# Kernel optimization log

Measured on AMD Instinct MI355X. Metric: run time of the kernel, lower is better.

The kernel has to match this reference:

```python
import jax, jax.numpy as jnp
import numpy as np

N_NODES = 10000
N_EDGES = 160000
D_IN = 512
D_OUT = 512


def setup_inputs() -> dict:
    key = jax.random.key(0)
    k_x, k_e, k_wl, k_wr = jax.random.split(key, 4)
    x = jax.random.normal(k_x, (N_NODES, D_IN), dtype=jnp.float32)
    edge_index = jax.random.randint(k_e, (2, N_EDGES), 0, N_NODES, dtype=jnp.int64)
    scale = 1.0 / np.sqrt(D_IN)
    W_l = jax.random.normal(k_wl, (D_IN, D_OUT), dtype=jnp.float32) * scale
    W_r = jax.random.normal(k_wr, (D_IN, D_OUT), dtype=jnp.float32) * scale
    b = jnp.zeros((D_OUT,), dtype=jnp.float32)
    return {"x": x, "edge_index": edge_index, "W_l": W_l, "W_r": W_r, "b": b}


def reference(x, edge_index, W_l, W_r, b):
    # dropout p=0.0 -> identity
    src = edge_index[0]  # message sources (x_j)
    dst = edge_index[1]  # aggregation targets (i)
    n = x.shape[0]
    # mean neighbor aggregation: scatter-add messages, divide by in-degree
    msg = x[src]                                   # [E, D_in]
    agg = jax.ops.segment_sum(msg, dst, num_segments=n)        # [N, D_in]
    deg = jax.ops.segment_sum(jnp.ones((src.shape[0],), x.dtype), dst, num_segments=n)
    mean = agg / jnp.maximum(deg, 1.0)[:, None]
    # SAGEConv: lin_l(aggregated) + lin_r(root), bias in lin_l
    h = mean @ W_l + b + x @ W_r                   # [N, D_out]
    # Swish activation
    return h * jax.nn.sigmoid(h)
```

## Files before the change

kernel.cpp:

```cpp
#include <hip/hip_runtime.h>
#include <cstdint>
#include <cstddef>

typedef unsigned short ushort_t;
typedef __attribute__((ext_vector_type(8))) short short8;
typedef __attribute__((ext_vector_type(4))) float float4_;
typedef __attribute__((ext_vector_type(2))) float float2_;

#define GLOBAL_AS __attribute__((address_space(1)))
#define LDS_AS    __attribute__((address_space(3)))

#define D_FEAT 512
#define KDIM   1024
#define CAP    80
#define BK     128

__device__ __forceinline__ ushort_t f2bf(float f) {
    union { float f; unsigned int i; } v; v.f = f;
    unsigned int x = v.i;
    unsigned int r = (x + 0x7fffu + ((x >> 16) & 1u)) >> 16;
    return (ushort_t)r;
}

__device__ __forceinline__ void accq(float* acc, uint2 v) {
    float2_ a01 = __builtin_amdgcn_cvt_pk_f32_fp8(v.x, false);
    float2_ a23 = __builtin_amdgcn_cvt_pk_f32_fp8(v.x, true);
    float2_ a45 = __builtin_amdgcn_cvt_pk_f32_fp8(v.y, false);
    float2_ a67 = __builtin_amdgcn_cvt_pk_f32_fp8(v.y, true);
    acc[0] += a01.x; acc[1] += a01.y;
    acc[2] += a23.x; acc[3] += a23.y;
    acc[4] += a45.x; acc[5] += a45.y;
    acc[6] += a67.x; acc[7] += a67.y;
}

__global__ __launch_bounds__(256) void prep_kernel(
    const float* __restrict__ Wl, const float* __restrict__ Wr,
    const float* __restrict__ x, const int* __restrict__ ei,
    ushort_t* __restrict__ BT, ushort_t* __restrict__ xb,
    unsigned char* __restrict__ xq, unsigned int* __restrict__ cnt,
    int* __restrict__ colbuf, int N, int E, int nchunks, int cb) {
    int b = blockIdx.x;
    int t = threadIdx.x;
    if (b < cb) {
        int idx = b * 256 + t;
        if (idx >= nchunks) return;
        int row = idx >> 7;
        int c = (idx & 127) << 2;
        float4 v = *(const float4*)&x[(size_t)row * D_FEAT + c];
        ushort_t o[4] = {f2bf(v.x), f2bf(v.y), f2bf(v.z), f2bf(v.w)};
        *(uint2*)&xb[(size_t)row * D_FEAT + c] = *(const uint2*)o;
        int pk = 0;
        pk = __builtin_amdgcn_cvt_pk_fp8_f32(v.x, v.y, pk, false);
        pk = __builtin_amdgcn_cvt_pk_fp8_f32(v.z, v.w, pk, true);
        *(int*)&xq[(size_t)row * D_FEAT + c] = pk;
    } else if (b < cb + 128) {
        int bb = b - cb;
        __shared__ float tile[64][68];
        int kb = (bb & 15) * 64, nb = (bb >> 4) * 64;
#pragma unroll
        for (int ph = 0; ph < 4; ++ph) {
            int f = t * 4 + ph * 1024;
            int k = f >> 6, n = f & 63;
            int gk = kb + k;
            const float* W = (gk < 512) ? (Wl + (size_t)gk * 512 + nb + n)
                                        : (Wr + (size_t)(gk - 512) * 512 + nb + n);
            *(float4*)&tile[k][n] = *(const float4*)W;
        }
        __syncthreads();
#pragma unroll
        for (int ph = 0; ph < 4; ++ph) {
            int f = t * 4 + ph * 1024;
            int n = f >> 6, k = f & 63;
            ushort_t tmp[4];
#pragma unroll
            for (int j = 0; j < 4; ++j) tmp[j] = f2bf(tile[k + j][n]);
            *(uint2*)&BT[(size_t)(nb + n) * KDIM + kb + k] = *(const uint2*)tmp;
        }
    } else {
        int e = ((b - cb - 128) * 256 + t) * 2;
        if (e >= E) return;
        unsigned int V = cnt[N];
        int2 d2 = *(const int2*)&ei[E + e];
        int2 s2 = *(const int2*)&ei[e];
        unsigned int p0 = atomicAdd(&cnt[d2.x], 1u) - V;
        if (p0 < CAP) colbuf[(size_t)d2.x * CAP + p0] = s2.x;
        if (e + 1 < E) {
            unsigned int p1 = atomicAdd(&cnt[d2.y], 1u) - V;
            if (p1 < CAP) colbuf[(size_t)d2.y * CAP + p1] = s2.y;
        }
    }
}

__global__ __launch_bounds__(256) void agg_kernel(
    const unsigned char* __restrict__ xq, ushort_t* __restrict__ mb,
    const unsigned int* __restrict__ cnt, const int* __restrict__ colbuf,
    int n) {
    int w = threadIdx.x >> 6, l = threadIdx.x & 63;
    int node = blockIdx.x * 4 + w;
    if (node >= n) return;
    unsigned int V = cnt[n];
    int f = l << 3;
    const unsigned char* gsrc = xq + f;
    const int* bucket = colbuf + (size_t)node * CAP;
    float acc[8] = {0.f, 0.f, 0.f, 0.f, 0.f, 0.f, 0.f, 0.f};
    int deg = (int)(cnt[node] - V);
    int e = deg < CAP ? deg : CAP;
    int j = 0;
    for (; j + 7 < e; j += 8) {
        int4 i0 = *(const int4*)&bucket[j];
        int4 i1 = *(const int4*)&bucket[j + 4];
        uint2 v0 = *(const uint2*)(gsrc + (size_t)i0.x * D_FEAT);
        uint2 v1 = *(const uint2*)(gsrc + (size_t)i0.y * D_FEAT);
        uint2 v2 = *(const uint2*)(gsrc + (size_t)i0.z * D_FEAT);
        uint2 v3 = *(const uint2*)(gsrc + (size_t)i0.w * D_FEAT);
        uint2 v4 = *(const uint2*)(gsrc + (size_t)i1.x * D_FEAT);
        uint2 v5 = *(const uint2*)(gsrc + (size_t)i1.y * D_FEAT);
        uint2 v6 = *(const uint2*)(gsrc + (size_t)i1.z * D_FEAT);
        uint2 v7 = *(const uint2*)(gsrc + (size_t)i1.w * D_FEAT);
        accq(acc, v0); accq(acc, v1); accq(acc, v2); accq(acc, v3);
        accq(acc, v4); accq(acc, v5); accq(acc, v6); accq(acc, v7);
    }
    if (j + 3 < e) {
        int4 i0 = *(const int4*)&bucket[j];
        uint2 v0 = *(const uint2*)(gsrc + (size_t)i0.x * D_FEAT);
        uint2 v1 = *(const uint2*)(gsrc + (size_t)i0.y * D_FEAT);
        uint2 v2 = *(const uint2*)(gsrc + (size_t)i0.z * D_FEAT);
        uint2 v3 = *(const uint2*)(gsrc + (size_t)i0.w * D_FEAT);
        accq(acc, v0); accq(acc, v1); accq(acc, v2); accq(acc, v3);
        j += 4;
    }
    for (; j < e; ++j) {
        uint2 v0 = *(const uint2*)(gsrc + (size_t)bucket[j] * D_FEAT);
        accq(acc, v0);
    }
    float scale = 1.0f / (float)(deg > 1 ? deg : 1);
    ushort_t o[8];
#pragma unroll
    for (int k = 0; k < 8; ++k) o[k] = f2bf(acc[k] * scale);
    *(uint4*)&mb[(size_t)node * D_FEAT + f] = *(const uint4*)o;
}

__global__ __launch_bounds__(256) void gemm_kernel(
    const ushort_t* __restrict__ mb, const ushort_t* __restrict__ xb,
    const ushort_t* __restrict__ BT, const float* __restrict__ bias,
    float* __restrict__ out, int nrows, int mpx) {
    __shared__ ushort_t As[128 * BK];
    __shared__ ushort_t Bs[64 * BK];
    int b = blockIdx.x;
    int xcd = b & 7, j = b >> 3;
    int tile_m = (xcd * mpx + (j >> 3)) * 128;
    int tile_n = (j & 7) * 64;
    int tid = threadIdx.x;
    int l = tid & 63;
    int w = tid >> 6;
    int lm = l & 15, q = l >> 4;
    int wm = (w >> 1) * 64, wn = (w & 1) * 32;

    float4_ acc[4][2];
#pragma unroll
    for (int i = 0; i < 4; ++i)
#pragma unroll
        for (int jj = 0; jj < 2; ++jj) acc[i][jj] = (float4_)(0.f);

    for (int k0 = 0; k0 < KDIM; k0 += BK) {
        const ushort_t* Asrc = (k0 < 512) ? mb : xb;
        int kk = k0 & 511;
#pragma unroll
        for (int cc = 0; cc < 8; ++cc) {
            int c = tid + cc * 256;
            int row = c >> 4;
            int kc = (c & 15) ^ (row & 15);
            const ushort_t* gp =
                Asrc + (size_t)(tile_m + row) * D_FEAT + kk + kc * 8;
            __builtin_amdgcn_global_load_lds(
                (const GLOBAL_AS unsigned int*)gp,
                (LDS_AS unsigned int*)&As[c * 8], 16, 0, 0);
        }
#pragma unroll
        for (int cc = 0; cc < 4; ++cc) {
            int c = tid + cc * 256;
            int row = c >> 4;
            int kc = (c & 15) ^ (row & 15);
            const ushort_t* gq =
                BT + (size_t)(tile_n + row) * KDIM + k0 + kc * 8;
            __builtin_amdgcn_global_load_lds(
                (const GLOBAL_AS unsigned int*)gq,
                (LDS_AS unsigned int*)&Bs[c * 8], 16, 0, 0);
        }
        __syncthreads();

#pragma unroll
        for (int s = 0; s < 4; ++s) {
            int kc = s * 4 + q;
            short8 a[4], bb[2];
#pragma unroll
            for (int i = 0; i < 4; ++i) {
                int row = wm + i * 16 + lm;
                a[i] = *(const short8*)&As[row * BK + ((kc ^ (row & 15)) << 3)];
            }
#pragma unroll
            for (int jj = 0; jj < 2; ++jj) {
                int col = wn + jj * 16 + lm;
                bb[jj] = *(const short8*)&Bs[col * BK + ((kc ^ (col & 15)) << 3)];
            }
#pragma unroll
            for (int i = 0; i < 4; ++i)
#pragma unroll
                for (int jj = 0; jj < 2; ++jj)
                    acc[i][jj] = __builtin_amdgcn_mfma_f32_16x16x32_bf16(
                        a[i], bb[jj], acc[i][jj], 0, 0, 0);
        }
        __syncthreads();
    }

#pragma unroll
    for (int jj = 0; jj < 2; ++jj) {
        int gcol = tile_n + wn + jj * 16 + lm;
        float bv = bias[gcol];
#pragma unroll
        for (int i = 0; i < 4; ++i) {
#pragma unroll
            for (int r = 0; r < 4; ++r) {
                int grow = tile_m + wm + i * 16 + q * 4 + r;
                if (grow < nrows) {
                    float h = acc[i][jj][r] + bv;
                    float sw = h / (1.f + __expf(-h));
                    out[(size_t)grow * D_FEAT + gcol] = sw;
                }
            }
        }
    }
}

extern "C" void kernel_launch(void* const* d_in, const int* in_sizes, int n_in,
                              void* d_out, int out_size, void* d_ws, size_t ws_size,
                              hipStream_t stream) {
    const float* x    = (const float*)d_in[0];
    const int*   ei   = (const int*)d_in[1];
    const float* Wl   = (const float*)d_in[2];
    const float* Wr   = (const float*)d_in[3];
    const float* bias = (const float*)d_in[4];
    float* out = (float*)d_out;

    const int N = in_sizes[0] / D_FEAT;
    const int E = in_sizes[1] / 2;
    int mt = (N + 127) / 128;
    mt = (mt + 7) & ~7;
    const int M_PAD = mt * 128;
    const int mpx = mt / 8;

    char* ws = (char*)d_ws;
    size_t off = 0;
    auto take = [&](size_t bytes) -> char* {
        char* p = ws + off;
        off += (bytes + 255) & ~(size_t)255;
        return p;
    };
    ushort_t*      xb     = (ushort_t*)take((size_t)M_PAD * D_FEAT * 2);
    ushort_t*      mb     = (ushort_t*)take((size_t)M_PAD * D_FEAT * 2);
    ushort_t*      BT     = (ushort_t*)take((size_t)D_FEAT * KDIM * 2);
    unsigned char* xq     = (unsigned char*)take((size_t)M_PAD * D_FEAT);
    unsigned int*  cnt    = (unsigned int*)take((size_t)M_PAD * 4);
    int*           colbuf = (int*)take((size_t)M_PAD * CAP * 4);

    int nchunks = N * (D_FEAT / 4);
    int cb = (nchunks + 255) / 256;
    int eb = (E / 2 + 255) / 256;
    prep_kernel<<<cb + 128 + eb, 256, 0, stream>>>(
        Wl, Wr, x, ei, BT, xb, xq, cnt, colbuf, N, E, nchunks, cb);

    agg_kernel<<<(N + 3) / 4, 256, 0, stream>>>(xq, mb, cnt, colbuf, N);

    gemm_kernel<<<mt * 8, 256, 0, stream>>>(mb, xb, BT, bias, out, N, mpx);
}
```

Baseline: 128.5 us.

## Double-buffer GEMM LDS tiles with BK=64 to overlap loads and MFMA

Halves the K tile to 64 and allocates two LDS buffers for the A and B tiles. The next tile's global-to-LDS loads are issued before computing on the current one, and a single barrier per iteration replaces two. This aims to hide global load latency behind MFMA work. In exchange the loop runs twice as many iterations, and the XOR swizzle shrinks from 16 chunks to 8.

```diff
diff --git a/kernel.cpp b/kernel.cpp
--- a/kernel.cpp
+++ b/kernel.cpp
@@ -13,7 +13,7 @@
 #define D_FEAT 512
 #define KDIM   1024
 #define CAP    80
-#define BK     128
+#define BK     64
 
 __device__ __forceinline__ ushort_t f2bf(float f) {
     union { float f; unsigned int i; } v; v.f = f;
@@ -144,8 +144,8 @@
     const ushort_t* __restrict__ mb, const ushort_t* __restrict__ xb,
     const ushort_t* __restrict__ BT, const float* __restrict__ bias,
     float* __restrict__ out, int nrows, int mpx) {
-    __shared__ ushort_t As[128 * BK];
-    __shared__ ushort_t Bs[64 * BK];
+    __shared__ ushort_t As[2][128 * BK];
+    __shared__ ushort_t Bs[2][64 * BK];
     int b = blockIdx.x;
     int xcd = b & 7, j = b >> 3;
     int tile_m = (xcd * mpx + (j >> 3)) * 128;
@@ -162,46 +162,46 @@
 #pragma unroll
         for (int jj = 0; jj < 2; ++jj) acc[i][jj] = (float4_)(0.f);
 
-    for (int k0 = 0; k0 < KDIM; k0 += BK) {
-        const ushort_t* Asrc = (k0 < 512) ? mb : xb;
-        int kk = k0 & 511;
-#pragma unroll
-        for (int cc = 0; cc < 8; ++cc) {
+    auto stage = [&](const ushort_t* Asrc, int kkA, int k0, ushort_t* Ad,
+                     ushort_t* Bd) {
+#pragma unroll
+        for (int cc = 0; cc < 4; ++cc) {
             int c = tid + cc * 256;
-            int row = c >> 4;
-            int kc = (c & 15) ^ (row & 15);
+            int row = c >> 3;
+            int kc = (c & 7) ^ (row & 7);
             const ushort_t* gp =
-                Asrc + (size_t)(tile_m + row) * D_FEAT + kk + kc * 8;
+                Asrc + (size_t)(tile_m + row) * D_FEAT + kkA + kc * 8;
             __builtin_amdgcn_global_load_lds(
                 (const GLOBAL_AS unsigned int*)gp,
-                (LDS_AS unsigned int*)&As[c * 8], 16, 0, 0);
-        }
-#pragma unroll
-        for (int cc = 0; cc < 4; ++cc) {
+                (LDS_AS unsigned int*)&Ad[c * 8], 16, 0, 0);
+        }
+#pragma unroll
+        for (int cc = 0; cc < 2; ++cc) {
             int c = tid + cc * 256;
-            int row = c >> 4;
-            int kc = (c & 15) ^ (row & 15);
+            int row = c >> 3;
+            int kc = (c & 7) ^ (row & 7);
             const ushort_t* gq =
                 BT + (size_t)(tile_n + row) * KDIM + k0 + kc * 8;
             __builtin_amdgcn_global_load_lds(
                 (const GLOBAL_AS unsigned int*)gq,
-                (LDS_AS unsigned int*)&Bs[c * 8], 16, 0, 0);
-        }
-        __syncthreads();
-
-#pragma unroll
-        for (int s = 0; s < 4; ++s) {
+                (LDS_AS unsigned int*)&Bd[c * 8], 16, 0, 0);
+        }
+    };
+
+    auto compute = [&](const ushort_t* A, const ushort_t* B) {
+#pragma unroll
+        for (int s = 0; s < 2; ++s) {
             int kc = s * 4 + q;
             short8 a[4], bb[2];
 #pragma unroll
             for (int i = 0; i < 4; ++i) {
                 int row = wm + i * 16 + lm;
-                a[i] = *(const short8*)&As[row * BK + ((kc ^ (row & 15)) << 3)];
+                a[i] = *(const short8*)&A[row * BK + ((kc ^ (row & 7)) << 3)];
             }
 #pragma unroll
             for (int jj = 0; jj < 2; ++jj) {
                 int col = wn + jj * 16 + lm;
-                bb[jj] = *(const short8*)&Bs[col * BK + ((kc ^ (col & 15)) << 3)];
+                bb[jj] = *(const short8*)&B[col * BK + ((kc ^ (col & 7)) << 3)];
             }
 #pragma unroll
             for (int i = 0; i < 4; ++i)
@@ -210,8 +210,24 @@
                     acc[i][jj] = __builtin_amdgcn_mfma_f32_16x16x32_bf16(
                         a[i], bb[jj], acc[i][jj], 0, 0, 0);
         }
+    };
+
+    ushort_t *Ac = As[0], *An = As[1], *Bc = Bs[0], *Bn = Bs[1];
+    stage(mb, 0, 0, Ac, Bc);
+    __syncthreads();
+
+#pragma unroll 1
+    for (int t = 0; t < (KDIM / BK) - 1; ++t) {
+        int k1 = (t + 1) * BK;
+        const ushort_t* Asrc = (k1 < 512) ? mb : xb;
+        stage(Asrc, k1 & 511, k1, An, Bn);
+        compute(Ac, Bc);
         __syncthreads();
-    }
+        ushort_t* tp;
+        tp = Ac; Ac = An; An = tp;
+        tp = Bc; Bc = Bn; Bn = tp;
+    }
+    compute(Ac, Bc);
 
 #pragma unroll
     for (int jj = 0; jj < 2; ++jj) {
```

After: 128.5 us (median of 2 runs). Within noise of the previous version (-0.0%).
